# Kernel optimization log

Hardware: AMD Instinct MI355X
Metric: run time of the kernel (lower is better)

Reference implementation:

```python
import jax, jax.numpy as jnp
import numpy as np

B, T, D = 2, 2048, 2048
H, LAT, RD = 16, 512, 64
HD = D // H  # 128


def _rope_tables(rd, max_t, theta=10000.0):
    freqs = 1.0 / theta ** (np.arange(0, rd, 2, dtype=np.float32) / rd)
    t = np.arange(max_t, dtype=np.float32)
    ang = np.outer(t, freqs)                      # (T, rd/2)
    cos = np.tile(np.cos(ang), (1, 2))            # (T, rd), matches torch .repeat(1,2)
    sin = np.tile(np.sin(ang), (1, 2))
    return jnp.asarray(cos), jnp.asarray(sin)


def _rotate_half(x):
    d = x.shape[-1] // 2
    return jnp.concatenate([-x[..., d:], x[..., :d]], axis=-1)


def _apply_rope(x, cos, sin):
    # x: (B, H, T, rd); cos/sin: (T, rd) broadcast over B, H
    t = x.shape[2]
    return x * cos[:t][None, None] + _rotate_half(x) * sin[:t][None, None]


def setup_inputs() -> dict:
    key = jax.random.key(0)
    ks = jax.random.split(key, 9)
    s = 0.02  # init scale to keep logits sane
    return {
        "x": jax.random.normal(ks[0], (B, T, D), jnp.float32),
        "Wqd": jax.random.normal(ks[1], (D, LAT), jnp.float32) * s,
        "Wqu": jax.random.normal(ks[2], (LAT, D), jnp.float32) * s,
        "Wqr": jax.random.normal(ks[3], (LAT, H * RD), jnp.float32) * s,
        "Wkvd": jax.random.normal(ks[4], (D, LAT), jnp.float32) * s,
        "Wku": jax.random.normal(ks[5], (LAT, D), jnp.float32) * s,
        "Wvu": jax.random.normal(ks[6], (LAT, D), jnp.float32) * s,
        "Wkr": jax.random.normal(ks[7], (D, RD), jnp.float32) * s,
        "Wo": jax.random.normal(ks[8], (D, D), jnp.float32) * s,
    }


def reference(x, Wqd, Wqu, Wqr, Wkvd, Wku, Wvu, Wkr, Wo):
    b, t, d = x.shape
    cos, sin = _rope_tables(RD, t)

    ql = x @ Wqd                                            # (B,T,LAT)
    q = (ql @ Wqu).reshape(b, t, H, HD).transpose(0, 2, 1, 3)      # (B,H,T,hd)
    qr = (ql @ Wqr).reshape(b, t, H, RD).transpose(0, 2, 1, 3)     # (B,H,T,rd)
    qr = _apply_rope(qr, cos, sin)

    ckv = x @ Wkvd                                          # (B,T,LAT)
    k = (ckv @ Wku).reshape(b, t, H, HD).transpose(0, 2, 1, 3)     # (B,H,T,hd)
    v = (ckv @ Wvu).reshape(b, t, H, HD).transpose(0, 2, 1, 3)     # (B,H,T,hd)

    kr = _apply_rope((x @ Wkr)[:, None], cos, sin)[:, 0]    # (B,T,rd), shared over heads

    scale = 1.0 / jnp.sqrt(jnp.float32(HD + RD))
    scores = (jnp.einsum('bhtd,bhsd->bhts', q, k)
              + jnp.einsum('bhtd,bsd->bhts', qr, kr)) * scale       # (B,H,T,T)

    causal = jnp.tril(jnp.ones((t, t), dtype=bool))
    scores = jnp.where(causal[None, None], scores, jnp.float32(-jnp.inf))
    attn = jax.nn.softmax(scores, axis=-1)

    out = jnp.einsum('bhts,bhsd->bhtd', attn, v)            # (B,H,T,hd)
    out = out.transpose(0, 2, 1, 3).reshape(b, t, d)        # (B,T,D)
    return out @ Wo
```

## Files before the change

kernel.cpp:

```cpp
#include <hip/hip_runtime.h>
#include <cmath>

typedef unsigned short ushort;
typedef __bf16 bf16x8 __attribute__((ext_vector_type(8)));
typedef float f32x4 __attribute__((ext_vector_type(4)));
typedef float f32x16 __attribute__((ext_vector_type(16)));
typedef unsigned int uint4v __attribute__((ext_vector_type(4)));
typedef unsigned int u2v __attribute__((ext_vector_type(2)));
typedef unsigned short ushort4v __attribute__((ext_vector_type(4)));

#define BB 2
#define TT 2048
#define DD 2048
#define HH 16
#define LATD 512
#define RDD 64
#define HDD 128
#define BT 4096
#define LDQ 2048
#define LDK 4096
#define LD1 1088

__device__ __forceinline__ ushort f2bf(float f) {
  union { float f; unsigned u; } v; v.f = f;
  return (ushort)((v.u + 0x7fffu + ((v.u >> 16) & 1u)) >> 16);
}
__device__ __forceinline__ float bf2f(ushort u) {
  union { unsigned u; float f; } v; v.u = ((unsigned)u) << 16; return v.f;
}
__device__ __forceinline__ f32x4 f4zero() {
  f32x4 v; v[0] = 0.f; v[1] = 0.f; v[2] = 0.f; v[3] = 0.f; return v;
}
__device__ __forceinline__ unsigned pkbf(float a, float b) {
  unsigned r;
  asm("v_cvt_pk_bf16_f32 %0, %1, %2" : "=v"(r) : "v"(a), "v"(b));
  return r;
}
__device__ __forceinline__ u2v pl32(unsigned a, unsigned b) {
  return __builtin_amdgcn_permlane32_swap(a, b, false, false);
}
__device__ __forceinline__ float xswap32(float v, int hl) {
  union { float f; unsigned u; } a; a.f = v;
  u2v r = pl32(a.u, a.u);
  union { unsigned u; float f; } o; o.u = hl ? r[0] : r[1];
  return o.f;
}

typedef __attribute__((address_space(1))) void g_void;
typedef __attribute__((address_space(3))) void l_void;
__device__ __forceinline__ void gld16(void* lds, const void* g) {
  __builtin_amdgcn_global_load_lds((g_void*)(unsigned long long)g, (l_void*)lds, 16, 0, 0);
}

__global__ void k_prep(const float* __restrict__ x, ushort* __restrict__ xb,
                       float* __restrict__ cosT, float* __restrict__ sinT,
                       const float* __restrict__ Wqd, const float* __restrict__ Wkvd,
                       const float* __restrict__ Wkr, const float* __restrict__ Wqu,
                       const float* __restrict__ Wqr, const float* __restrict__ Wku,
                       const float* __restrict__ Wvu, const float* __restrict__ Wo,
                       ushort* __restrict__ w1T, ushort* __restrict__ w2T,
                       ushort* __restrict__ w3T, ushort* __restrict__ woT) {
  __shared__ float t[32][33];
  int bid = blockIdx.x, tid = threadIdx.x;
  if (bid < 8192) {
    int i = bid * 256 + tid;
    f32x4 v = *(const f32x4*)(x + (size_t)i * 4);
    ushort4v u;
#pragma unroll
    for (int r = 0; r < 4; ++r) u[r] = f2bf(v[r]);
    *(ushort4v*)(xb + (size_t)i * 4) = u;
    return;
  }
  if (bid < 8448) {
    int i = (bid - 8192) * 256 + tid;
    int tt = i >> 5, jj = i & 31;
    float freq = exp2f(-(float)jj * (13.287712379549449f / 32.0f));
    float ang = (float)tt * freq;
    float s, c;
    sincosf(ang, &s, &c);
    cosT[i] = c; sinT[i] = s;
    return;
  }
  bid -= 8448;
  const float* in; ushort* out; int R, C, gx;
  if (bid < 1024)      { in = Wqd;  out = w1T;                          R = 2048; C = 512;  gx = 16; }
  else if (bid < 2048) { in = Wkvd; out = w1T + (size_t)512 * 2048;     R = 2048; C = 512;  gx = 16; bid -= 1024; }
  else if (bid < 2176) { in = Wkr;  out = w1T + (size_t)1024 * 2048;    R = 2048; C = 64;   gx = 2;  bid -= 2048; }
  else if (bid < 3200) { in = Wqu;  out = w2T;                          R = 512;  C = 2048; gx = 64; bid -= 2176; }
  else if (bid < 3712) { in = Wqr;  out = w2T + (size_t)2048 * 512;     R = 512;  C = 1024; gx = 32; bid -= 3200; }
  else if (bid < 4736) { in = Wku;  out = w3T;                          R = 512;  C = 2048; gx = 64; bid -= 3712; }
  else if (bid < 5760) { in = Wvu;  out = w3T + (size_t)2048 * 512;     R = 512;  C = 2048; gx = 64; bid -= 4736; }
  else                 { in = Wo;   out = woT;                          R = 2048; C = 2048; gx = 64; bid -= 5760; }
  int c0 = (bid % gx) * 32, r0 = (bid / gx) * 32;
  int tx = tid & 31, ty = tid >> 5;
#pragma unroll
  for (int i = 0; i < 4; ++i)
    t[ty + i * 8][tx] = in[(size_t)(r0 + ty + i * 8) * C + c0 + tx];
  __syncthreads();
#pragma unroll
  for (int i = 0; i < 4; ++i)
    out[(size_t)(c0 + ty + i * 8) * R + r0 + tx] = f2bf(t[tx][ty + i * 8]);
}

__global__ void k_vt(const ushort* __restrict__ in, ushort* __restrict__ out) {
  __shared__ ushort tile[32][33];
  int bh = blockIdx.z, b = bh >> 4, h = bh & 15;
  int t0 = blockIdx.x * 32, d0 = blockIdx.y * 32;
  int tx = threadIdx.x, ty = threadIdx.y;
#pragma unroll
  for (int i = 0; i < 4; ++i)
    tile[ty + i * 8][tx] = in[(size_t)(b * TT + t0 + ty + i * 8) * LDK + h * HDD + d0 + tx];
  __syncthreads();
#pragma unroll
  for (int i = 0; i < 4; ++i)
    out[(size_t)(bh * HDD + d0 + ty + i * 8) * TT + t0 + tx] = tile[tx][ty + i * 8];
}

template <typename OutT>
__global__ __launch_bounds__(256) void k_gemm(const ushort* __restrict__ A,
                                              const ushort* __restrict__ Bt,
                                              OutT* __restrict__ C,
                                              int M, int N, int K, int lda, int ldc, float alpha) {
  __shared__ __align__(16) ushort As[128 * 64];
  __shared__ __align__(16) ushort Bs[128 * 64];
  int tid = threadIdx.x;
  int lane = tid & 63, wid = tid >> 6;
  int wm = wid >> 1, wn = wid & 1;
  int lo = lane & 15, hi = lane >> 4;
  int m0 = blockIdx.y * 128, n0 = blockIdx.x * 128;
  int lr = lane >> 3, lc = (lane & 7) * 8;
  f32x4 acc[4][4];
#pragma unroll
  for (int m = 0; m < 4; ++m)
#pragma unroll
    for (int n = 0; n < 4; ++n) acc[m][n] = f4zero();

  for (int k0 = 0; k0 < K; k0 += 64) {
    __syncthreads();
#pragma unroll
    for (int it = 0; it < 4; ++it) {
      int c = wid * 4 + it;
      int row = c * 8 + lr;
      gld16(As + c * 512, A + (size_t)(m0 + row) * lda + k0 + lc);
      gld16(Bs + c * 512, Bt + (size_t)(n0 + row) * K + k0 + lc);
    }
    __syncthreads();
#pragma unroll
    for (int kk = 0; kk < 2; ++kk) {
      bf16x8 af[4], bfr[4];
#pragma unroll
      for (int m = 0; m < 4; ++m)
        af[m] = *(const bf16x8*)(As + (wm * 64 + m * 16 + lo) * 64 + kk * 32 + hi * 8);
#pragma unroll
      for (int n = 0; n < 4; ++n)
        bfr[n] = *(const bf16x8*)(Bs + (wn * 64 + n * 16 + lo) * 64 + kk * 32 + hi * 8);
      __builtin_amdgcn_s_setprio(1);
#pragma unroll
      for (int m = 0; m < 4; ++m)
#pragma unroll
        for (int n = 0; n < 4; ++n)
          acc[m][n] = __builtin_amdgcn_mfma_f32_16x16x32_bf16(af[m], bfr[n], acc[m][n], 0, 0, 0);
      __builtin_amdgcn_s_setprio(0);
    }
  }
#pragma unroll
  for (int m = 0; m < 4; ++m)
#pragma unroll
    for (int n = 0; n < 4; ++n)
#pragma unroll
      for (int r = 0; r < 4; ++r) {
        int row = m0 + wm * 64 + m * 16 + hi * 4 + r;
        int col = n0 + wn * 64 + n * 16 + lo;
        if (col < N) {
          float v = acc[m][n][r] * alpha;
          if constexpr (sizeof(OutT) == 4) C[(size_t)row * ldc + col] = v;
          else C[(size_t)row * ldc + col] = f2bf(v);
        }
      }
}

__global__ __launch_bounds__(256) void k_gemm1(const ushort* __restrict__ A, const ushort* __restrict__ Bt,
                                               ushort* __restrict__ C, ushort* __restrict__ Kr,
                                               const float* __restrict__ cosT, const float* __restrict__ sinT) {
  __shared__ __align__(16) ushort As[128 * 64];
  __shared__ __align__(16) ushort Bs[128 * 64];
  const int K = DD, lda = DD, ldc = LD1;
  int tid = threadIdx.x;
  int lane = tid & 63, wid = tid >> 6;
  int wm = wid >> 1, wn = wid & 1;
  int lo = lane & 15, hi = lane >> 4;
  int m0 = blockIdx.y * 128, n0 = blockIdx.x * 128;
  int bx = blockIdx.x;
  int lr = lane >> 3, lc = (lane & 7) * 8;
  f32x4 acc[4][4];
#pragma unroll
  for (int m = 0; m < 4; ++m)
#pragma unroll
    for (int n = 0; n < 4; ++n) acc[m][n] = f4zero();

  for (int k0 = 0; k0 < K; k0 += 64) {
    __syncthreads();
#pragma unroll
    for (int it = 0; it < 4; ++it) {
      int c = wid * 4 + it;
      int row = c * 8 + lr;
      gld16(As + c * 512, A + (size_t)(m0 + row) * lda + k0 + lc);
      gld16(Bs + c * 512, Bt + (size_t)(n0 + row) * K + k0 + lc);
    }
    __syncthreads();
#pragma unroll
    for (int kk = 0; kk < 2; ++kk) {
      bf16x8 af[4], bfr[4];
#pragma unroll
      for (int m = 0; m < 4; ++m)
        af[m] = *(const bf16x8*)(As + (wm * 64 + m * 16 + lo) * 64 + kk * 32 + hi * 8);
#pragma unroll
      for (int n = 0; n < 4; ++n)
        bfr[n] = *(const bf16x8*)(Bs + (wn * 64 + n * 16 + lo) * 64 + kk * 32 + hi * 8);
      __builtin_amdgcn_s_setprio(1);
#pragma unroll
      for (int m = 0; m < 4; ++m)
#pragma unroll
        for (int n = 0; n < 4; ++n)
          acc[m][n] = __builtin_amdgcn_mfma_f32_16x16x32_bf16(af[m], bfr[n], acc[m][n], 0, 0, 0);
      __builtin_amdgcn_s_setprio(0);
    }
  }
  if (bx < 8) {
#pragma unroll
    for (int m = 0; m < 4; ++m)
#pragma unroll
      for (int n = 0; n < 4; ++n)
#pragma unroll
        for (int r = 0; r < 4; ++r) {
          int row = m0 + wm * 64 + m * 16 + hi * 4 + r;
          int col = n0 + wn * 64 + n * 16 + lo;
          C[(size_t)row * ldc + col] = f2bf(acc[m][n][r]);
        }
  } else if (wn == 0) {
#pragma unroll
    for (int m = 0; m < 4; ++m)
#pragma unroll
      for (int r = 0; r < 4; ++r) {
        int row = m0 + wm * 64 + m * 16 + hi * 4 + r;
        int t = row & (TT - 1);
        float c0 = cosT[t * 32 + lo],      s0 = sinT[t * 32 + lo];
        float c1 = cosT[t * 32 + 16 + lo], s1 = sinT[t * 32 + 16 + lo];
        float x0 = acc[m][0][r], x1 = acc[m][1][r];
        float x2 = acc[m][2][r], x3 = acc[m][3][r];
        size_t base = (size_t)row * 64 + lo;
        Kr[base +  0] = f2bf(x0 * c0 - x2 * s0);
        Kr[base + 16] = f2bf(x1 * c1 - x3 * s1);
        Kr[base + 32] = f2bf(x2 * c0 + x0 * s0);
        Kr[base + 48] = f2bf(x3 * c1 + x1 * s1);
      }
  }
}

__global__ __launch_bounds__(256) void k_gemm23(const ushort* __restrict__ A1, const ushort* __restrict__ B1,
                                                ushort* __restrict__ Cq, ushort* __restrict__ Cr,
                                                const ushort* __restrict__ A2, const ushort* __restrict__ B2,
                                                ushort* __restrict__ Ckv, float a1,
                                                const float* __restrict__ cosT, const float* __restrict__ sinT) {
  __shared__ __align__(16) ushort As[128 * 64];
  __shared__ __align__(16) ushort Bs[128 * 64];
  int bx = blockIdx.x;
  const ushort* A; const ushort* Bt; int n0;
  if (bx < 24) { A = A1; Bt = B1; n0 = bx * 128; }
  else         { A = A2; Bt = B2; n0 = (bx - 24) * 128; }
  const int K = LATD, lda = LD1;
  int tid = threadIdx.x;
  int lane = tid & 63, wid = tid >> 6;
  int wm = wid >> 1, wn = wid & 1;
  int lo = lane & 15, hi = lane >> 4;
  int m0 = blockIdx.y * 128;
  int lr = lane >> 3, lc = (lane & 7) * 8;
  f32x4 acc[4][4];
#pragma unroll
  for (int m = 0; m < 4; ++m)
#pragma unroll
    for (int n = 0; n < 4; ++n) acc[m][n] = f4zero();

  for (int k0 = 0; k0 < K; k0 += 64) {
    __syncthreads();
#pragma unroll
    for (int it = 0; it < 4; ++it) {
      int c = wid * 4 + it;
      int row = c * 8 + lr;
      gld16(As + c * 512, A + (size_t)(m0 + row) * lda + k0 + lc);
      gld16(Bs + c * 512, Bt + (size_t)(n0 + row) * K + k0 + lc);
    }
    __syncthreads();
#pragma unroll
    for (int kk = 0; kk < 2; ++kk) {
      bf16x8 af[4], bfr[4];
#pragma unroll
      for (int m = 0; m < 4; ++m)
        af[m] = *(const bf16x8*)(As + (wm * 64 + m * 16 + lo) * 64 + kk * 32 + hi * 8);
#pragma unroll
      for (int n = 0; n < 4; ++n)
        bfr[n] = *(const bf16x8*)(Bs + (wn * 64 + n * 16 + lo) * 64 + kk * 32 + hi * 8);
      __builtin_amdgcn_s_setprio(1);
#pragma unroll
      for (int m = 0; m < 4; ++m)
#pragma unroll
        for (int n = 0; n < 4; ++n)
          acc[m][n] = __builtin_amdgcn_mfma_f32_16x16x32_bf16(af[m], bfr[n], acc[m][n], 0, 0, 0);
      __builtin_amdgcn_s_setprio(0);
    }
  }
  if (bx < 16) {
#pragma unroll
    for (int m = 0; m < 4; ++m)
#pragma unroll
      for (int n = 0; n < 4; ++n)
#pragma unroll
        for (int r = 0; r < 4; ++r) {
          int row = m0 + wm * 64 + m * 16 + hi * 4 + r;
          int col = n0 + wn * 64 + n * 16 + lo;
          Cq[(size_t)row * 2048 + col] = f2bf(acc[m][n][r] * a1);
        }
  } else if (bx < 24) {
#pragma unroll
    for (int m = 0; m < 4; ++m)
#pragma unroll
      for (int r = 0; r < 4; ++r) {
        int row = m0 + wm * 64 + m * 16 + hi * 4 + r;
        int t = row & (TT - 1);
        float c0 = cosT[t * 32 + lo],      s0 = sinT[t * 32 + lo];
        float c1 = cosT[t * 32 + 16 + lo], s1 = sinT[t * 32 + 16 + lo];
        float x0 = acc[m][0][r], x1 = acc[m][1][r];
        float x2 = acc[m][2][r], x3 = acc[m][3][r];
        size_t base = (size_t)row * 1024 + (bx - 16) * 128 + wn * 64 + lo;
        Cr[base +  0] = f2bf((x0 * c0 - x2 * s0) * a1);
        Cr[base + 16] = f2bf((x1 * c1 - x3 * s1) * a1);
        Cr[base + 32] = f2bf((x2 * c0 + x0 * s0) * a1);
        Cr[base + 48] = f2bf((x3 * c1 + x1 * s1) * a1);
      }
  } else {
#pragma unroll
    for (int m = 0; m < 4; ++m)
#pragma unroll
      for (int n = 0; n < 4; ++n)
#pragma unroll
        for (int r = 0; r < 4; ++r) {
          int row = m0 + wm * 64 + m * 16 + hi * 4 + r;
          int col = n0 + wn * 64 + n * 16 + lo;
          Ckv[(size_t)row * 4096 + col] = f2bf(acc[m][n][r]);
        }
  }
}

__global__ __launch_bounds__(256, 2) void k_attn(const ushort* __restrict__ qb, const ushort* __restrict__ qrb,
                                                 const ushort* __restrict__ kb, const ushort* __restrict__ krb,
                                                 const ushort* __restrict__ vt, ushort* __restrict__ ao) {
  __shared__ __align__(16) ushort SH[24576];
#define KS(buf) (SH + (buf) * 8192)
#define KR(buf) (SH + 16384 + (buf) * 4096)
  const int tid = threadIdx.x, lane = tid & 63, w = tid >> 6;
  const int cq = lane & 31;
  const int hl = lane >> 5;
  const int lin = (int)blockIdx.x + 16 * (int)blockIdx.y + 256 * (int)blockIdx.z;
  const int combo = lin & 31;
  const int pr = lin >> 5, h = combo & 15, b = combo >> 4;
  const int tA = pr, tB = 31 - pr;
  const int nch = tB + 1;
  const int myTile = (w >= 2) ? tB : tA;
  const int myDiag = myTile;
  const int qrow = myTile * 64 + (w & 1) * 32 + cq;
  const int swzK = (cq & 15) << 3;
  const int swzR = (cq & 7) << 3;

  bf16x8 qf[12];
  {
    const ushort* qp = qb + (size_t)(b * TT + qrow) * LDQ + h * HDD;
#pragma unroll
    for (int f = 0; f < 8; ++f) qf[f] = *(const bf16x8*)(qp + f * 16 + hl * 8);
    const ushort* qrp = qrb + (size_t)(b * TT + qrow) * 1024 + h * RDD;
#pragma unroll
    for (int f = 0; f < 4; ++f) qf[8 + f] = *(const bf16x8*)(qrp + f * 16 + hl * 8);
  }
  f32x16 o0, o1, o2, o3;
#pragma unroll
  for (int r = 0; r < 16; ++r) { o0[r] = 0.f; o1[r] = 0.f; o2[r] = 0.f; o3[r] = 0.f; }
  float m = -__builtin_inff(), l = 0.f;

  auto stage = [&](int buf, int kb0) {
#pragma unroll
    for (int it = 0; it < 4; ++it) {
      int cb = (tid & ~63) + it * 256;
      int c = cb + lane;
      int row = c >> 4;
      int ccg = (c & 15) ^ (row & 15);
      gld16(&KS(buf)[cb * 8], kb + (size_t)(b * TT + kb0 + row) * LDK + h * HDD + ccg * 8);
    }
#pragma unroll
    for (int it = 0; it < 2; ++it) {
      int cb = (tid & ~63) + it * 256;
      int c = cb + lane;
      int row = c >> 3;
      int ccg = (c & 7) ^ (row & 7);
      gld16(&KR(buf)[cb * 8], krb + (size_t)(b * TT + kb0 + row) * RDD + ccg * 8);
    }
  };

  stage(0, 0);
  __syncthreads();

  const ushort* vth = vt + (size_t)(b * HH + h) * HDD * TT;

  int cur = 0;
  for (int ch = 0; ch < nch; ++ch) {
    const int kb0 = ch * 64;
    if (ch + 1 < nch) stage(cur ^ 1, kb0 + 64);

    if (ch <= myDiag) {
      f32x16 s0, s1;
#pragma unroll
      for (int r = 0; r < 16; ++r) { s0[r] = 0.f; s1[r] = 0.f; }
      __builtin_amdgcn_s_setprio(1);
#pragma unroll
      for (int f = 0; f < 12; ++f) {
        const ushort* base = (f < 8) ? KS(cur) : KR(cur);
        const int stride = (f < 8) ? 128 : 64;
        const int colU = ((f < 8) ? f * 16 : (f - 8) * 16) + hl * 8;
        const int sz = (f < 8) ? swzK : swzR;
        bf16x8 k0 = *(const bf16x8*)(base + cq * stride + (colU ^ sz));
        bf16x8 k1 = *(const bf16x8*)(base + (32 + cq) * stride + (colU ^ sz));
        s0 = __builtin_amdgcn_mfma_f32_32x32x16_bf16(k0, qf[f], s0, 0, 0, 0);
        s1 = __builtin_amdgcn_mfma_f32_32x32x16_bf16(k1, qf[f], s1, 0, 0, 0);
      }
      __builtin_amdgcn_s_setprio(0);

      float mx = -__builtin_inff();
      if (ch == myDiag) {
#pragma unroll
        for (int r = 0; r < 16; ++r) {
          int kp = kb0 + (r & 3) + 8 * (r >> 2) + 4 * hl;
          if (kp > qrow) s0[r] = -__builtin_inff();
          mx = fmaxf(mx, s0[r]);
          if (kp + 32 > qrow) s1[r] = -__builtin_inff();
          mx = fmaxf(mx, s1[r]);
        }
      } else {
#pragma unroll
        for (int r = 0; r < 16; ++r) mx = fmaxf(fmaxf(mx, s0[r]), s1[r]);
      }
      mx = fmaxf(mx, xswap32(mx, hl));

      uint4v va[4], vb2[4];
      {
        const ushort* vp = vth + (size_t)(0 * 32 + cq) * TT + kb0 + hl * 8;
        va[0] = *(const uint4v*)(vp);
        va[1] = *(const uint4v*)(vp + 16);
        va[2] = *(const uint4v*)(vp + 32);
        va[3] = *(const uint4v*)(vp + 48);
      }

      bool defer = __all(mx <= m + 8.f);
      float mnew = defer ? m : fmaxf(m, mx);
      float rs = 0.f;
#pragma unroll
      for (int r = 0; r < 16; ++r) {
        s0[r] = exp2f(s0[r] - mnew); rs += s0[r];
        s1[r] = exp2f(s1[r] - mnew); rs += s1[r];
      }
      rs += xswap32(rs, hl);
      if (!defer) {
        float al = exp2f(m - mnew);
#pragma unroll
        for (int r = 0; r < 16; ++r) { o0[r] *= al; o1[r] *= al; o2[r] *= al; o3[r] *= al; }
        l = l * al + rs;
        m = mnew;
      } else {
        l += rs;
      }

      bf16x8 pf0, pf1, pf2, pf3;
#define PBUILD(PF, S, RB)                                                   \
      {                                                                     \
        unsigned a2 = pkbf(S[RB + 0], S[RB + 1]);                           \
        unsigned b2 = pkbf(S[RB + 2], S[RB + 3]);                           \
        unsigned c2 = pkbf(S[RB + 4], S[RB + 5]);                           \
        unsigned d2 = pkbf(S[RB + 6], S[RB + 7]);                           \
        u2v r02 = pl32(a2, c2);                                             \
        u2v r13 = pl32(b2, d2);                                             \
        union { uint4v u; bf16x8 v; } pb_;                                  \
        pb_.u[0] = r02[0];                                                  \
        pb_.u[1] = r13[0];                                                  \
        pb_.u[2] = r02[1];                                                  \
        pb_.u[3] = r13[1];                                                  \
        PF = pb_.v;                                                         \
      }
      PBUILD(pf0, s0, 0)
      PBUILD(pf1, s0, 8)
      PBUILD(pf2, s1, 0)
      PBUILD(pf3, s1, 8)
#undef PBUILD

#define VLOAD(DST, DT)                                                      \
      {                                                                     \
        const ushort* vp = vth + (size_t)((DT) * 32 + cq) * TT + kb0 + hl * 8;\
        DST[0] = *(const uint4v*)(vp);                                      \
        DST[1] = *(const uint4v*)(vp + 16);                                 \
        DST[2] = *(const uint4v*)(vp + 32);                                 \
        DST[3] = *(const uint4v*)(vp + 48);                                 \
      }
#define PVSTEP(OD, VS)                                                      \
      {                                                                     \
        union { uint4v u; bf16x8 v; } cv_;                                  \
        __builtin_amdgcn_s_setprio(1);                                      \
        cv_.u = VS[0]; OD = __builtin_amdgcn_mfma_f32_32x32x16_bf16(cv_.v, pf0, OD, 0, 0, 0); \
        cv_.u = VS[1]; OD = __builtin_amdgcn_mfma_f32_32x32x16_bf16(cv_.v, pf1, OD, 0, 0, 0); \
        cv_.u = VS[2]; OD = __builtin_amdgcn_mfma_f32_32x32x16_bf16(cv_.v, pf2, OD, 0, 0, 0); \
        cv_.u = VS[3]; OD = __builtin_amdgcn_mfma_f32_32x32x16_bf16(cv_.v, pf3, OD, 0, 0, 0); \
        __builtin_amdgcn_s_setprio(0);                                      \
      }
      VLOAD(vb2, 1)
      PVSTEP(o0, va)
      VLOAD(va, 2)
      PVSTEP(o1, vb2)
      VLOAD(vb2, 3)
      PVSTEP(o2, va)
      PVSTEP(o3, vb2)
#undef VLOAD
#undef PVSTEP
    }

    __syncthreads();
    cur ^= 1;
  }

  float inv = 1.0f / l;
  const int ebase = w * 4352;
#define OSPILL(OD, DT)                                                      \
  _Pragma("unroll")                                                         \
  for (int g = 0; g < 4; ++g) {                                             \
    ushort4v u;                                                             \
    _Pragma("unroll")                                                       \
    for (int j = 0; j < 4; ++j) u[j] = f2bf(OD[g * 4 + j] * inv);           \
    *(ushort4v*)(&SH[ebase + cq * 136 + (DT) * 32 + g * 8 + hl * 4]) = u;   \
  }
  OSPILL(o0, 0)
  OSPILL(o1, 1)
  OSPILL(o2, 2)
  OSPILL(o3, 3)
#undef OSPILL
  {
    const size_t rbase = (size_t)(b * TT + myTile * 64 + (w & 1) * 32);
#pragma unroll
    for (int p = 0; p < 8; ++p) {
      int q = p * 4 + (lane >> 4);
      uint4v v = *(const uint4v*)(&SH[ebase + q * 136 + (lane & 15) * 8]);
      *(uint4v*)(&ao[(rbase + q) * DD + h * HDD + (lane & 15) * 8]) = v;
    }
  }
#undef KS
#undef KR
}

extern "C" void kernel_launch(void* const* d_in, const int* in_sizes, int n_in,
                              void* d_out, int out_size, void* d_ws, size_t ws_size,
                              hipStream_t stream) {
  (void)in_sizes; (void)n_in; (void)out_size; (void)ws_size;
  const float* x    = (const float*)d_in[0];
  const float* Wqd  = (const float*)d_in[1];
  const float* Wqu  = (const float*)d_in[2];
  const float* Wqr  = (const float*)d_in[3];
  const float* Wkvd = (const float*)d_in[4];
  const float* Wku  = (const float*)d_in[5];
  const float* Wvu  = (const float*)d_in[6];
  const float* Wkr  = (const float*)d_in[7];
  const float* Wo   = (const float*)d_in[8];
  float* out = (float*)d_out;

  char* ws = (char*)d_ws;
  size_t off = 0;
  auto alloc = [&](size_t bytes) { void* p = ws + off; off += (bytes + 255) & ~(size_t)255; return p; };
  ushort* xb   = (ushort*)alloc((size_t)BT * DD * 2);
  ushort* w1T  = (ushort*)alloc((size_t)(LD1 + 64) * DD * 2);
  ushort* w2T  = (ushort*)alloc((size_t)3072 * LATD * 2);
  ushort* w3T  = (ushort*)alloc((size_t)4096 * LATD * 2);
  ushort* woT  = (ushort*)alloc((size_t)DD * DD * 2);
  ushort* xc   = (ushort*)alloc((size_t)BT * LD1 * 2);
  ushort* qqr  = (ushort*)alloc((size_t)BT * 2048 * 2);
  ushort* kv   = (ushort*)alloc((size_t)BT * 4096 * 2);
  ushort* qrB  = (ushort*)alloc((size_t)BT * 1024 * 2);
  ushort* krB  = (ushort*)alloc((size_t)BT * RDD * 2);
  ushort* vtB  = (ushort*)alloc((size_t)BT * DD * 2);
  ushort* aoB  = (ushort*)alloc((size_t)BT * DD * 2);
  float*  cosT = (float*)alloc((size_t)TT * 32 * 4);
  float*  sinT = (float*)alloc((size_t)TT * 32 * 4);

  float qscale = 1.4426950408889634f / sqrtf(192.0f);

  k_prep<<<dim3(18304), 256, 0, stream>>>(x, xb, cosT, sinT,
                                          Wqd, Wkvd, Wkr, Wqu, Wqr, Wku, Wvu, Wo,
                                          w1T, w2T, w3T, woT);

  k_gemm1<<<dim3(9, BT / 128), 256, 0, stream>>>(xb, w1T, xc, krB, cosT, sinT);
  k_gemm23<<<dim3(56, BT / 128), 256, 0, stream>>>(xc, w2T, qqr, qrB, xc + 512, w3T, kv,
                                                   qscale, cosT, sinT);

  k_vt<<<dim3(TT / 32, HDD / 32, BB * HH), dim3(32, 8), 0, stream>>>(kv + 2048, vtB);

  k_attn<<<dim3(16, HH, BB), 256, 0, stream>>>(qqr, qrB, kv, krB, vtB, aoB);

  k_gemm<float><<<dim3(16, BT / 128), 256, 0, stream>>>(aoB, woT, out, BT, DD, DD, DD, DD, 1.0f);
}
```

Measured before the change: 282.7 us.

## Fuse V transpose into projection GEMM epilogue and software-pipeline PV in attention

Result: slower. 317.6 us (+12.4%).

```diff
diff --git a/kernel.cpp b/kernel.cpp
--- a/kernel.cpp
+++ b/kernel.cpp
@@ -18,7 +18,7 @@
 #define HDD 128
 #define BT 4096
 #define LDQ 2048
-#define LDK 4096
+#define LDK 2048
 #define LD1 1088
 
 __device__ __forceinline__ ushort f2bf(float f) {
@@ -102,20 +102,6 @@
     out[(size_t)(c0 + ty + i * 8) * R + r0 + tx] = f2bf(t[tx][ty + i * 8]);
 }
 
-__global__ void k_vt(const ushort* __restrict__ in, ushort* __restrict__ out) {
-  __shared__ ushort tile[32][33];
-  int bh = blockIdx.z, b = bh >> 4, h = bh & 15;
-  int t0 = blockIdx.x * 32, d0 = blockIdx.y * 32;
-  int tx = threadIdx.x, ty = threadIdx.y;
-#pragma unroll
-  for (int i = 0; i < 4; ++i)
-    tile[ty + i * 8][tx] = in[(size_t)(b * TT + t0 + ty + i * 8) * LDK + h * HDD + d0 + tx];
-  __syncthreads();
-#pragma unroll
-  for (int i = 0; i < 4; ++i)
-    out[(size_t)(bh * HDD + d0 + ty + i * 8) * TT + t0 + tx] = tile[tx][ty + i * 8];
-}
-
 template <typename OutT>
 __global__ __launch_bounds__(256) void k_gemm(const ushort* __restrict__ A,
                                               const ushort* __restrict__ Bt,
@@ -260,10 +246,11 @@
 __global__ __launch_bounds__(256) void k_gemm23(const ushort* __restrict__ A1, const ushort* __restrict__ B1,
                                                 ushort* __restrict__ Cq, ushort* __restrict__ Cr,
                                                 const ushort* __restrict__ A2, const ushort* __restrict__ B2,
-                                                ushort* __restrict__ Ckv, float a1,
+                                                ushort* __restrict__ Ck, ushort* __restrict__ Vt, float a1,
                                                 const float* __restrict__ cosT, const float* __restrict__ sinT) {
-  __shared__ __align__(16) ushort As[128 * 64];
-  __shared__ __align__(16) ushort Bs[128 * 64];
+  __shared__ __align__(16) ushort SH[128 * 128];
+  ushort* As = SH;
+  ushort* Bs = SH + 8192;
   int bx = blockIdx.x;
   const ushort* A; const ushort* Bt; int n0;
   if (bx < 24) { A = A1; Bt = B1; n0 = bx * 128; }
@@ -337,7 +324,7 @@
         Cr[base + 32] = f2bf((x2 * c0 + x0 * s0) * a1);
         Cr[base + 48] = f2bf((x3 * c1 + x1 * s1) * a1);
       }
-  } else {
+  } else if (bx < 40) {
 #pragma unroll
     for (int m = 0; m < 4; ++m)
 #pragma unroll
@@ -346,14 +333,40 @@
         for (int r = 0; r < 4; ++r) {
           int row = m0 + wm * 64 + m * 16 + hi * 4 + r;
           int col = n0 + wn * 64 + n * 16 + lo;
-          Ckv[(size_t)row * 4096 + col] = f2bf(acc[m][n][r]);
+          Ck[(size_t)row * 2048 + col] = f2bf(acc[m][n][r]);
         }
-  }
-}
-
-__global__ __launch_bounds__(256, 2) void k_attn(const ushort* __restrict__ qb, const ushort* __restrict__ qrb,
-                                                 const ushort* __restrict__ kb, const ushort* __restrict__ krb,
-                                                 const ushort* __restrict__ vt, ushort* __restrict__ ao) {
+  } else {
+    __syncthreads();
+#pragma unroll
+    for (int m = 0; m < 4; ++m)
+#pragma unroll
+      for (int n = 0; n < 4; ++n) {
+        int col = wn * 64 + n * 16 + lo;
+#pragma unroll
+        for (int r = 0; r < 4; ++r) {
+          int row = wm * 64 + m * 16 + hi * 4 + r;
+          SH[col * 128 + (row ^ ((col & 15) << 3))] = f2bf(acc[m][n][r]);
+        }
+      }
+    __syncthreads();
+    int hh = bx - 40;
+    int b = m0 >> 11, tt0 = m0 & 2047;
+    const size_t vbase = ((size_t)(b * HH + hh) * HDD) * TT + tt0;
+#pragma unroll
+    for (int it = 0; it < 8; ++it) {
+      int idx = it * 256 + tid;
+      int col = idx >> 4;
+      int r8 = (idx & 15) * 8;
+      uint4v v = *(const uint4v*)(&SH[col * 128 + (r8 ^ ((col & 15) << 3))]);
+      *(uint4v*)(&Vt[vbase + (size_t)col * TT + r8]) = v;
+    }
+  }
+}
+
+__global__ __attribute__((amdgpu_flat_work_group_size(256, 256), amdgpu_waves_per_eu(2, 2)))
+void k_attn(const ushort* __restrict__ qb, const ushort* __restrict__ qrb,
+            const ushort* __restrict__ kb, const ushort* __restrict__ krb,
+            const ushort* __restrict__ vt, ushort* __restrict__ ao) {
   __shared__ __align__(16) ushort SH[24576];
 #define KS(buf) (SH + (buf) * 8192)
 #define KR(buf) (SH + 16384 + (buf) * 4096)
@@ -409,12 +422,38 @@
 
   const ushort* vth = vt + (size_t)(b * HH + h) * HDD * TT;
 
+#define VLOAD(DST, DT, KB)                                                  \
+  {                                                                         \
+    const ushort* vp = vth + (size_t)((DT) * 32 + cq) * TT + (KB) + hl * 8; \
+    DST[0] = *(const uint4v*)(vp);                                          \
+    DST[1] = *(const uint4v*)(vp + 16);                                     \
+    DST[2] = *(const uint4v*)(vp + 32);                                     \
+    DST[3] = *(const uint4v*)(vp + 48);                                     \
+  }
+#define PVSTEP(OD, VS)                                                      \
+  {                                                                         \
+    union { uint4v u; bf16x8 v; } cv_;                                      \
+    __builtin_amdgcn_s_setprio(1);                                          \
+    cv_.u = VS[0]; OD = __builtin_amdgcn_mfma_f32_32x32x16_bf16(cv_.v, pf0, OD, 0, 0, 0); \
+    cv_.u = VS[1]; OD = __builtin_amdgcn_mfma_f32_32x32x16_bf16(cv_.v, pf1, OD, 0, 0, 0); \
+    cv_.u = VS[2]; OD = __builtin_amdgcn_mfma_f32_32x32x16_bf16(cv_.v, pf2, OD, 0, 0, 0); \
+    cv_.u = VS[3]; OD = __builtin_amdgcn_mfma_f32_32x32x16_bf16(cv_.v, pf3, OD, 0, 0, 0); \
+    __builtin_amdgcn_s_setprio(0);                                          \
+  }
+
+  bf16x8 pf0, pf1, pf2, pf3;
+  bool havePrev = false;
+  int pvKb0 = 0;
+
   int cur = 0;
   for (int ch = 0; ch < nch; ++ch) {
     const int kb0 = ch * 64;
     if (ch + 1 < nch) stage(cur ^ 1, kb0 + 64);
 
     if (ch <= myDiag) {
+      uint4v va[4], vb2[4];
+      if (havePrev) { VLOAD(va, 0, pvKb0) VLOAD(vb2, 1, pvKb0) }
+
       f32x16 s0, s1;
 #pragma unroll
       for (int r = 0; r < 16; ++r) { s0[r] = 0.f; s1[r] = 0.f; }
@@ -432,6 +471,15 @@
       }
       __builtin_amdgcn_s_setprio(0);
 
+      if (havePrev) {
+        PVSTEP(o0, va)
+        VLOAD(va, 2, pvKb0)
+        PVSTEP(o1, vb2)
+        VLOAD(vb2, 3, pvKb0)
+        PVSTEP(o2, va)
+        PVSTEP(o3, vb2)
+      }
+
       float mx = -__builtin_inff();
       if (ch == myDiag) {
 #pragma unroll
@@ -448,15 +496,6 @@
       }
       mx = fmaxf(mx, xswap32(mx, hl));
 
-      uint4v va[4], vb2[4];
-      {
-        const ushort* vp = vth + (size_t)(0 * 32 + cq) * TT + kb0 + hl * 8;
-        va[0] = *(const uint4v*)(vp);
-        va[1] = *(const uint4v*)(vp + 16);
-        va[2] = *(const uint4v*)(vp + 32);
-        va[3] = *(const uint4v*)(vp + 48);
-      }
-
       bool defer = __all(mx <= m + 8.f);
       float mnew = defer ? m : fmaxf(m, mx);
       float rs = 0.f;
@@ -476,7 +515,6 @@
         l += rs;
       }
 
-      bf16x8 pf0, pf1, pf2, pf3;
 #define PBUILD(PF, S, RB)                                                   \
       {                                                                     \
         unsigned a2 = pkbf(S[RB + 0], S[RB + 1]);                           \
@@ -497,39 +535,27 @@
       PBUILD(pf2, s1, 0)
       PBUILD(pf3, s1, 8)
 #undef PBUILD
-
-#define VLOAD(DST, DT)                                                      \
-      {                                                                     \
-        const ushort* vp = vth + (size_t)((DT) * 32 + cq) * TT + kb0 + hl * 8;\
-        DST[0] = *(const uint4v*)(vp);                                      \
-        DST[1] = *(const uint4v*)(vp + 16);                                 \
-        DST[2] = *(const uint4v*)(vp + 32);                                 \
-        DST[3] = *(const uint4v*)(vp + 48);                                 \
-      }
-#define PVSTEP(OD, VS)                                                      \
-      {                                                                     \
-        union { uint4v u; bf16x8 v; } cv_;                                  \
-        __builtin_amdgcn_s_setprio(1);                                      \
-        cv_.u = VS[0]; OD = __builtin_amdgcn_mfma_f32_32x32x16_bf16(cv_.v, pf0, OD, 0, 0, 0); \
-        cv_.u = VS[1]; OD = __builtin_amdgcn_mfma_f32_32x32x16_bf16(cv_.v, pf1, OD, 0, 0, 0); \
-        cv_.u = VS[2]; OD = __builtin_amdgcn_mfma_f32_32x32x16_bf16(cv_.v, pf2, OD, 0, 0, 0); \
-        cv_.u = VS[3]; OD = __builtin_amdgcn_mfma_f32_32x32x16_bf16(cv_.v, pf3, OD, 0, 0, 0); \
-        __builtin_amdgcn_s_setprio(0);                                      \
-      }
-      VLOAD(vb2, 1)
-      PVSTEP(o0, va)
-      VLOAD(va, 2)
-      PVSTEP(o1, vb2)
-      VLOAD(vb2, 3)
-      PVSTEP(o2, va)
-      PVSTEP(o3, vb2)
+      pvKb0 = kb0;
+      havePrev = true;
+    }
+
+    __syncthreads();
+    cur ^= 1;
+  }
+
+  if (havePrev) {
+    uint4v va[4], vb2[4];
+    VLOAD(va, 0, pvKb0)
+    VLOAD(vb2, 1, pvKb0)
+    PVSTEP(o0, va)
+    VLOAD(va, 2, pvKb0)
+    PVSTEP(o1, vb2)
+    VLOAD(vb2, 3, pvKb0)
+    PVSTEP(o2, va)
+    PVSTEP(o3, vb2)
+  }
 #undef VLOAD
 #undef PVSTEP
-    }
-
-    __syncthreads();
-    cur ^= 1;
-  }
 
   float inv = 1.0f / l;
   const int ebase = w * 4352;
@@ -584,7 +610,7 @@
   ushort* woT  = (ushort*)alloc((size_t)DD * DD * 2);
   ushort* xc   = (ushort*)alloc((size_t)BT * LD1 * 2);
   ushort* qqr  = (ushort*)alloc((size_t)BT * 2048 * 2);
-  ushort* kv   = (ushort*)alloc((size_t)BT * 4096 * 2);
+  ushort* kB   = (ushort*)alloc((size_t)BT * 2048 * 2);
   ushort* qrB  = (ushort*)alloc((size_t)BT * 1024 * 2);
   ushort* krB  = (ushort*)alloc((size_t)BT * RDD * 2);
   ushort* vtB  = (ushort*)alloc((size_t)BT * DD * 2);
@@ -599,12 +625,10 @@
                                           w1T, w2T, w3T, woT);
 
   k_gemm1<<<dim3(9, BT / 128), 256, 0, stream>>>(xb, w1T, xc, krB, cosT, sinT);
-  k_gemm23<<<dim3(56, BT / 128), 256, 0, stream>>>(xc, w2T, qqr, qrB, xc + 512, w3T, kv,
-                                                   qscale, cosT, sinT);
-
-  k_vt<<<dim3(TT / 32, HDD / 32, BB * HH), dim3(32, 8), 0, stream>>>(kv + 2048, vtB);
-
-  k_attn<<<dim3(16, HH, BB), 256, 0, stream>>>(qqr, qrB, kv, krB, vtB, aoB);
+  k_gemm23<<<dim3(56, BT / 128), 256, 0, stream>>>(xc, w2T, qqr, qrB, xc + 512, w3T,
+                                                   kB, vtB, qscale, cosT, sinT);
+
+  k_attn<<<dim3(16, HH, BB), 256, 0, stream>>>(qqr, qrB, kB, krB, vtB, aoB);
 
   k_gemm<float><<<dim3(16, BT / 128), 256, 0, stream>>>(aoB, woT, out, BT, DD, DD, DD, DD, 1.0f);
 }
```

## Double-buffer LDS tiles in GEMM kernels to overlap global loads with MFMA

Applied to the files above, without the earlier changes.

New measurement: 273.8 us. 1.03x faster.

```diff
diff --git a/kernel.cpp b/kernel.cpp
--- a/kernel.cpp
+++ b/kernel.cpp
@@ -121,8 +121,8 @@
                                               const ushort* __restrict__ Bt,
                                               OutT* __restrict__ C,
                                               int M, int N, int K, int lda, int ldc, float alpha) {
-  __shared__ __align__(16) ushort As[128 * 64];
-  __shared__ __align__(16) ushort Bs[128 * 64];
+  __shared__ __align__(16) ushort As[2][128 * 64];
+  __shared__ __align__(16) ushort Bs[2][128 * 64];
   int tid = threadIdx.x;
   int lane = tid & 63, wid = tid >> 6;
   int wm = wid >> 1, wn = wid & 1;
@@ -135,25 +135,30 @@
 #pragma unroll
     for (int n = 0; n < 4; ++n) acc[m][n] = f4zero();
 
-  for (int k0 = 0; k0 < K; k0 += 64) {
-    __syncthreads();
+  auto stage = [&](int buf, int k0) {
 #pragma unroll
     for (int it = 0; it < 4; ++it) {
       int c = wid * 4 + it;
       int row = c * 8 + lr;
-      gld16(As + c * 512, A + (size_t)(m0 + row) * lda + k0 + lc);
-      gld16(Bs + c * 512, Bt + (size_t)(n0 + row) * K + k0 + lc);
-    }
-    __syncthreads();
+      gld16(As[buf] + c * 512, A + (size_t)(m0 + row) * lda + k0 + lc);
+      gld16(Bs[buf] + c * 512, Bt + (size_t)(n0 + row) * K + k0 + lc);
+    }
+  };
+
+  stage(0, 0);
+  __syncthreads();
+  int cur = 0;
+  for (int k0 = 0; k0 < K; k0 += 64) {
+    if (k0 + 64 < K) stage(cur ^ 1, k0 + 64);
 #pragma unroll
     for (int kk = 0; kk < 2; ++kk) {
       bf16x8 af[4], bfr[4];
 #pragma unroll
       for (int m = 0; m < 4; ++m)
-        af[m] = *(const bf16x8*)(As + (wm * 64 + m * 16 + lo) * 64 + kk * 32 + hi * 8);
+        af[m] = *(const bf16x8*)(As[cur] + (wm * 64 + m * 16 + lo) * 64 + kk * 32 + hi * 8);
 #pragma unroll
       for (int n = 0; n < 4; ++n)
-        bfr[n] = *(const bf16x8*)(Bs + (wn * 64 + n * 16 + lo) * 64 + kk * 32 + hi * 8);
+        bfr[n] = *(const bf16x8*)(Bs[cur] + (wn * 64 + n * 16 + lo) * 64 + kk * 32 + hi * 8);
       __builtin_amdgcn_s_setprio(1);
 #pragma unroll
       for (int m = 0; m < 4; ++m)
@@ -162,6 +167,8 @@
           acc[m][n] = __builtin_amdgcn_mfma_f32_16x16x32_bf16(af[m], bfr[n], acc[m][n], 0, 0, 0);
       __builtin_amdgcn_s_setprio(0);
     }
+    __syncthreads();
+    cur ^= 1;
   }
 #pragma unroll
   for (int m = 0; m < 4; ++m)
@@ -182,8 +189,8 @@
 __global__ __launch_bounds__(256) void k_gemm1(const ushort* __restrict__ A, const ushort* __restrict__ Bt,
                                                ushort* __restrict__ C, ushort* __restrict__ Kr,
                                                const float* __restrict__ cosT, const float* __restrict__ sinT) {
-  __shared__ __align__(16) ushort As[128 * 64];
-  __shared__ __align__(16) ushort Bs[128 * 64];
+  __shared__ __align__(16) ushort As[2][128 * 64];
+  __shared__ __align__(16) ushort Bs[2][128 * 64];
   const int K = DD, lda = DD, ldc = LD1;
   int tid = threadIdx.x;
   int lane = tid & 63, wid = tid >> 6;
@@ -198,25 +205,30 @@
 #pragma unroll
     for (int n = 0; n < 4; ++n) acc[m][n] = f4zero();
 
-  for (int k0 = 0; k0 < K; k0 += 64) {
-    __syncthreads();
+  auto stage = [&](int buf, int k0) {
 #pragma unroll
     for (int it = 0; it < 4; ++it) {
       int c = wid * 4 + it;
       int row = c * 8 + lr;
-      gld16(As + c * 512, A + (size_t)(m0 + row) * lda + k0 + lc);
-      gld16(Bs + c * 512, Bt + (size_t)(n0 + row) * K + k0 + lc);
-    }
-    __syncthreads();
+      gld16(As[buf] + c * 512, A + (size_t)(m0 + row) * lda + k0 + lc);
+      gld16(Bs[buf] + c * 512, Bt + (size_t)(n0 + row) * K + k0 + lc);
+    }
+  };
+
+  stage(0, 0);
+  __syncthreads();
+  int cur = 0;
+  for (int k0 = 0; k0 < K; k0 += 64) {
+    if (k0 + 64 < K) stage(cur ^ 1, k0 + 64);
 #pragma unroll
     for (int kk = 0; kk < 2; ++kk) {
       bf16x8 af[4], bfr[4];
 #pragma unroll
       for (int m = 0; m < 4; ++m)
-        af[m] = *(const bf16x8*)(As + (wm * 64 + m * 16 + lo) * 64 + kk * 32 + hi * 8);
+        af[m] = *(const bf16x8*)(As[cur] + (wm * 64 + m * 16 + lo) * 64 + kk * 32 + hi * 8);
 #pragma unroll
       for (int n = 0; n < 4; ++n)
-        bfr[n] = *(const bf16x8*)(Bs + (wn * 64 + n * 16 + lo) * 64 + kk * 32 + hi * 8);
+        bfr[n] = *(const bf16x8*)(Bs[cur] + (wn * 64 + n * 16 + lo) * 64 + kk * 32 + hi * 8);
       __builtin_amdgcn_s_setprio(1);
 #pragma unroll
       for (int m = 0; m < 4; ++m)
@@ -225,6 +237,8 @@
           acc[m][n] = __builtin_amdgcn_mfma_f32_16x16x32_bf16(af[m], bfr[n], acc[m][n], 0, 0, 0);
       __builtin_amdgcn_s_setprio(0);
     }
+    __syncthreads();
+    cur ^= 1;
   }
   if (bx < 8) {
 #pragma unroll
@@ -262,8 +276,8 @@
                                                 const ushort* __restrict__ A2, const ushort* __restrict__ B2,
                                                 ushort* __restrict__ Ckv, float a1,
                                                 const float* __restrict__ cosT, const float* __restrict__ sinT) {
-  __shared__ __align__(16) ushort As[128 * 64];
-  __shared__ __align__(16) ushort Bs[128 * 64];
+  __shared__ __align__(16) ushort As[2][128 * 64];
+  __shared__ __align__(16) ushort Bs[2][128 * 64];
   int bx = blockIdx.x;
   const ushort* A; const ushort* Bt; int n0;
   if (bx < 24) { A = A1; Bt = B1; n0 = bx * 128; }
@@ -281,25 +295,30 @@
 #pragma unroll
     for (int n = 0; n < 4; ++n) acc[m][n] = f4zero();
 
-  for (int k0 = 0; k0 < K; k0 += 64) {
-    __syncthreads();
+  auto stage = [&](int buf, int k0) {
 #pragma unroll
     for (int it = 0; it < 4; ++it) {
       int c = wid * 4 + it;
       int row = c * 8 + lr;
-      gld16(As + c * 512, A + (size_t)(m0 + row) * lda + k0 + lc);
-      gld16(Bs + c * 512, Bt + (size_t)(n0 + row) * K + k0 + lc);
-    }
-    __syncthreads();
+      gld16(As[buf] + c * 512, A + (size_t)(m0 + row) * lda + k0 + lc);
+      gld16(Bs[buf] + c * 512, Bt + (size_t)(n0 + row) * K + k0 + lc);
+    }
+  };
+
+  stage(0, 0);
+  __syncthreads();
+  int cur = 0;
+  for (int k0 = 0; k0 < K; k0 += 64) {
+    if (k0 + 64 < K) stage(cur ^ 1, k0 + 64);
 #pragma unroll
     for (int kk = 0; kk < 2; ++kk) {
       bf16x8 af[4], bfr[4];
 #pragma unroll
       for (int m = 0; m < 4; ++m)
-        af[m] = *(const bf16x8*)(As + (wm * 64 + m * 16 + lo) * 64 + kk * 32 + hi * 8);
+        af[m] = *(const bf16x8*)(As[cur] + (wm * 64 + m * 16 + lo) * 64 + kk * 32 + hi * 8);
 #pragma unroll
       for (int n = 0; n < 4; ++n)
-        bfr[n] = *(const bf16x8*)(Bs + (wn * 64 + n * 16 + lo) * 64 + kk * 32 + hi * 8);
+        bfr[n] = *(const bf16x8*)(Bs[cur] + (wn * 64 + n * 16 + lo) * 64 + kk * 32 + hi * 8);
       __builtin_amdgcn_s_setprio(1);
 #pragma unroll
       for (int m = 0; m < 4; ++m)
@@ -308,6 +327,8 @@
           acc[m][n] = __builtin_amdgcn_mfma_f32_16x16x32_bf16(af[m], bfr[n], acc[m][n], 0, 0, 0);
       __builtin_amdgcn_s_setprio(0);
     }
+    __syncthreads();
+    cur ^= 1;
   }
   if (bx < 16) {
 #pragma unroll
```
